# Kernel optimization log

Hardware: AMD Instinct MI355X
Metric: run time of the kernel (lower is better)

## Reference

```python
import math
import jax, jax.numpy as jnp
import numpy as np
from jax import lax

NUM_HEADS = 8


def _conv(x, w, b):
    # 3x3 same-padding conv, NCHW / OIHW
    y = lax.conv_general_dilated(x, w, (1, 1), ((1, 1), (1, 1)),
                                 dimension_numbers=("NCHW", "OIHW", "NCHW"))
    return y + b[None, :, None, None]


def setup_inputs() -> dict:
    key = jax.random.key(0)
    ks = jax.random.split(key, 9)
    C = 16
    s = 0.05
    inp = {"x": jax.random.normal(ks[0], (4, C, 256, 512), jnp.float32)}
    names = ["wq", "bq", "wk", "bk", "wv", "bv", "wo", "bo"]
    for i, n in enumerate(names):
        if n.startswith("w"):
            inp[n] = jax.random.normal(ks[i + 1], (C, C, 3, 3), jnp.float32) * s
        else:
            inp[n] = jax.random.normal(ks[i + 1], (C,), jnp.float32) * s
    return inp


def reference(x, wq, bq, wk, bk, wv, bv, wo, bo):
    b, c, h, w = x.shape
    d = h // NUM_HEADS  # per-head feature dim along the height axis

    def split_heads(t):  # (b,c,h,w) -> (b,c,heads,w,d)
        return t.transpose(0, 1, 3, 2).reshape(b, c, w, NUM_HEADS, d).transpose(0, 1, 3, 2, 4)

    q = split_heads(_conv(x, wq, bq)).astype(jnp.float32)
    k = split_heads(_conv(x, wk, bk)).astype(jnp.float32)
    v = split_heads(_conv(x, wv, bv)).astype(jnp.float32)

    # attention over the width (frame) axis, fp32, scaled by sqrt(h)
    qk = jnp.einsum("bcnwd,bcnud->bcnwu", q, k) / math.sqrt(h)
    a = jnp.einsum("bcnwu,bcnud->bcnwd", jax.nn.softmax(qk, axis=-1), v)

    # (b,c,heads,w,d) -> (b,c,w,h) -> (b,c,h,w)
    a = a.transpose(0, 1, 3, 2, 4).reshape(b, c, w, h).transpose(0, 1, 3, 2)
    return _conv(a, wo, bo)
```

## Files before the change

kernel.cpp:

```cpp
#include <hip/hip_runtime.h>

#define BB 4
#define CC 16
#define HH 256
#define WW 512
#define NHD 8
#define DD 32

typedef __attribute__((ext_vector_type(8))) short s8b;
typedef __attribute__((ext_vector_type(4))) float f32x4;
typedef __attribute__((ext_vector_type(4))) unsigned int u32x4;
typedef __attribute__((ext_vector_type(2))) int i32x2;

__device__ inline unsigned cvtpk(float a, float b) {
    unsigned r;
    asm("v_cvt_pk_bf16_f32 %0, %1, %2" : "=v"(r) : "v"(a), "v"(b));
    return r;
}
__device__ inline f32x4 mfma16(u32x4 a, u32x4 b, f32x4 c) {
    return __builtin_amdgcn_mfma_f32_16x16x32_bf16(
        __builtin_bit_cast(s8b, a), __builtin_bit_cast(s8b, b), c, 0, 0, 0);
}

__global__ __launch_bounds__(64)
void wsetup_kernel(const float* __restrict__ w0, const float* __restrict__ w1,
                   const float* __restrict__ w2, const float* __restrict__ w3,
                   unsigned* __restrict__ wfrag)
{
    const int lane = threadIdx.x;
    const int cv = blockIdx.x;
    const float* wg[4] = {w0, w1, w2, w3};
    const int r = lane & 15, g = lane >> 4;
    const int ci0 = (g & 1) * 8;
    #pragma unroll
    for (int kg = 0; kg < 5; ++kg) {
        int tap = 2*kg + (g >> 1);
        unsigned hi[4], lo[4];
        #pragma unroll
        for (int j = 0; j < 4; ++j) {
            float e0 = 0.f, e1 = 0.f;
            if (tap < 9) {
                e0 = wg[cv][(r*CC + ci0 + 2*j    )*9 + tap];
                e1 = wg[cv][(r*CC + ci0 + 2*j + 1)*9 + tap];
            }
            unsigned h = cvtpk(e0, e1);
            float f0 = __builtin_bit_cast(float, h << 16);
            float f1 = __builtin_bit_cast(float, h & 0xffff0000u);
            hi[j] = h;
            lo[j] = cvtpk(e0 - f0, e1 - f1);
        }
        *(u32x4*)(wfrag + (size_t)(((0*4 + cv)*5 + kg)*64 + lane)*4) =
            (u32x4){hi[0], hi[1], hi[2], hi[3]};
        *(u32x4*)(wfrag + (size_t)(((1*4 + cv)*5 + kg)*64 + lane)*4) =
            (u32x4){lo[0], lo[1], lo[2], lo[3]};
    }
}

template<int NC, int CVB, bool IN_PAIRED, bool OUT_PAIRED, int NTERM>
__global__ __launch_bounds__(256)
void conv_mfma_kernel(const void* __restrict__ xin,
                      const unsigned* __restrict__ wfrag,
                      const float* __restrict__ b0, const float* __restrict__ b1,
                      const float* __restrict__ b2,
                      unsigned* __restrict__ o0, unsigned* __restrict__ o1,
                      unsigned* __restrict__ o2, float* __restrict__ of,
                      float kscale)
{
    constexpr int LC2 = 34, NPX = 18*34;
    constexpr int PXB = (NTERM == 3) ? 64 : 32;
    __shared__ __align__(16) unsigned char xs[NPX*PXB];

    const int tid = threadIdx.x;
    const int bx = blockIdx.x, by = blockIdx.y, bz = blockIdx.z;
    const int lane = tid & 63, wid = tid >> 6;
    const int g = lane >> 4, r = lane & 15;

    u32x4 wh[NC][5], wl[NC][5];
    #pragma unroll
    for (int cv = 0; cv < NC; ++cv)
        #pragma unroll
        for (int kg = 0; kg < 5; ++kg) {
            wh[cv][kg] = *(const u32x4*)(wfrag + (size_t)(((CVB+cv)*5 + kg)*64 + lane)*4);
            if constexpr (NTERM >= 2)
                wl[cv][kg] = *(const u32x4*)(wfrag + (size_t)(((4+CVB+cv)*5 + kg)*64 + lane)*4);
        }
    const float* bg[3] = {b0, b1, b2};
    f32x4 bias[NC];
    #pragma unroll
    for (int cv = 0; cv < NC; ++cv) bias[cv] = *(const f32x4*)(bg[cv] + 4*g);

    const int row0 = by*16 - 1, col0 = bx*32 - 1;
    for (int idx = tid; idx < NPX; idx += 256) {
        int rr = idx / LC2, cc2 = idx - rr*LC2;
        int gr = row0 + rr, gc = col0 + cc2;
        bool ok = (gr >= 0) & (gr < HH) & (gc >= 0) & (gc < WW);
        unsigned hi[8];
        if constexpr (IN_PAIRED) {
            const unsigned* xb = (const unsigned*)xin + (size_t)bz*CC*(HH/2)*WW;
            int grc = gr < 0 ? 0 : (gr > HH-1 ? HH-1 : gr);
            int gcc = gc < 0 ? 0 : (gc > WW-1 ? WW-1 : gc);
            const unsigned* px = xb + (size_t)(grc >> 1)*WW + gcc;
            unsigned wv[16];
            #pragma unroll
            for (int c8 = 0; c8 < 16; ++c8)
                wv[c8] = ok ? px[(size_t)c8*(HH/2)*WW] : 0u;
            const unsigned sel = (grc & 1) ? 0x07060302u : 0x05040100u;
            #pragma unroll
            for (int p = 0; p < 8; ++p)
                hi[p] = __builtin_amdgcn_perm(wv[2*p+1], wv[2*p], sel);
        } else {
            const float* xb = (const float*)xin + (size_t)bz*CC*HH*WW;
            const float* px = xb + (size_t)gr*WW + gc;
            float v0[16];
            #pragma unroll
            for (int c8 = 0; c8 < 16; ++c8) v0[c8] = ok ? px[(size_t)c8*HH*WW] : 0.f;
            #pragma unroll
            for (int p = 0; p < 8; ++p) hi[p] = cvtpk(v0[2*p], v0[2*p+1]);
            if constexpr (NTERM == 3) {
                unsigned lo[8];
                #pragma unroll
                for (int p = 0; p < 8; ++p) {
                    float f0 = __builtin_bit_cast(float, hi[p] << 16);
                    float f1 = __builtin_bit_cast(float, hi[p] & 0xffff0000u);
                    lo[p] = cvtpk(v0[2*p] - f0, v0[2*p+1] - f1);
                }
                unsigned base = (unsigned)idx*64, m = ((unsigned)idx & 3) << 4;
                *(u32x4*)(xs + base + ((32u) ^ m)) = (u32x4){lo[0], lo[1], lo[2], lo[3]};
                *(u32x4*)(xs + base + ((48u) ^ m)) = (u32x4){lo[4], lo[5], lo[6], lo[7]};
            }
        }
        if constexpr (NTERM == 3) {
            unsigned base = (unsigned)idx*64, m = ((unsigned)idx & 3) << 4;
            *(u32x4*)(xs + base + (( 0u) ^ m)) = (u32x4){hi[0], hi[1], hi[2], hi[3]};
            *(u32x4*)(xs + base + ((16u) ^ m)) = (u32x4){hi[4], hi[5], hi[6], hi[7]};
        } else {
            unsigned base = (unsigned)idx*32, m = ((unsigned)idx & 4) << 2;
            *(u32x4*)(xs + base + (( 0u) ^ m)) = (u32x4){hi[0], hi[1], hi[2], hi[3]};
            *(u32x4*)(xs + base + ((16u) ^ m)) = (u32x4){hi[4], hi[5], hi[6], hi[7]};
        }
    }
    __syncthreads();

    int pk_base[5];
    #pragma unroll
    for (int kg = 0; kg < 5; ++kg) {
        int tap = 2*kg + (g >> 1);
        if (tap > 8) tap = 8;
        pk_base[kg] = (tap/3)*LC2 + (tap%3) + r;
    }
    const unsigned sh = (unsigned)(g & 1) << 4;

    auto tile = [&](int hr, int wt, f32x4* acc) {
        const int tb = hr*LC2 + wt*16;
        #pragma unroll
        for (int kg = 0; kg < 5; ++kg) {
            int px = tb + pk_base[kg];
            if constexpr (NTERM == 3) {
                unsigned b_ = (unsigned)px*64, m = ((unsigned)px & 3) << 4;
                u32x4 Bh = *(const u32x4*)(xs + b_ + ( sh        ^ m));
                u32x4 Bl = *(const u32x4*)(xs + b_ + ((sh | 32u) ^ m));
                #pragma unroll
                for (int cv = 0; cv < NC; ++cv) {
                    acc[cv] = mfma16(wh[cv][kg], Bh, acc[cv]);
                    acc[cv] = mfma16(wl[cv][kg], Bh, acc[cv]);
                    acc[cv] = mfma16(wh[cv][kg], Bl, acc[cv]);
                }
            } else {
                unsigned b_ = (unsigned)px*32, m = ((unsigned)px & 4) << 2;
                u32x4 Bh = *(const u32x4*)(xs + b_ + (sh ^ m));
                #pragma unroll
                for (int cv = 0; cv < NC; ++cv) {
                    acc[cv] = mfma16(wh[cv][kg], Bh, acc[cv]);
                    if constexpr (NTERM >= 2)
                        acc[cv] = mfma16(wl[cv][kg], Bh, acc[cv]);
                }
            }
        }
    };

    #pragma unroll 1
    for (int hp = 0; hp < 2; ++hp) {
        const int hrE = 4*wid + 2*hp;
        #pragma unroll 1
        for (int wt = 0; wt < 2; ++wt) {
            const int col = bx*32 + wt*16 + r;
            if constexpr (OUT_PAIRED) {
                f32x4 aE[NC];
                #pragma unroll
                for (int cv = 0; cv < NC; ++cv) aE[cv] = (f32x4){0.f,0.f,0.f,0.f};
                tile(hrE, wt, aE);
                unsigned Ep[NC][2];
                #pragma unroll
                for (int cv = 0; cv < NC; ++cv) {
                    const float sc = (cv == 1) ? kscale : 1.0f;
                    Ep[cv][0] = cvtpk((aE[cv][0] + bias[cv][0])*sc, (aE[cv][1] + bias[cv][1])*sc);
                    Ep[cv][1] = cvtpk((aE[cv][2] + bias[cv][2])*sc, (aE[cv][3] + bias[cv][3])*sc);
                }
                f32x4 aO[NC];
                #pragma unroll
                for (int cv = 0; cv < NC; ++cv) aO[cv] = (f32x4){0.f,0.f,0.f,0.f};
                tile(hrE + 1, wt, aO);
                const int hpix = by*8 + 2*wid + hp;
                #pragma unroll
                for (int cv = 0; cv < NC; ++cv) {
                    const float sc = (cv == 1) ? kscale : 1.0f;
                    unsigned Op0 = cvtpk((aO[cv][0] + bias[cv][0])*sc, (aO[cv][1] + bias[cv][1])*sc);
                    unsigned Op1 = cvtpk((aO[cv][2] + bias[cv][2])*sc, (aO[cv][3] + bias[cv][3])*sc);
                    unsigned wd[4] = {
                        __builtin_amdgcn_perm(Op0, Ep[cv][0], 0x05040100u),
                        __builtin_amdgcn_perm(Op0, Ep[cv][0], 0x07060302u),
                        __builtin_amdgcn_perm(Op1, Ep[cv][1], 0x05040100u),
                        __builtin_amdgcn_perm(Op1, Ep[cv][1], 0x07060302u) };
                    unsigned* op = (cv == 0) ? o0 : (cv == 1) ? o1 : o2;
                    #pragma unroll
                    for (int reg = 0; reg < 4; ++reg)
                        op[((size_t)(bz*CC + 4*g + reg)*(HH/2) + hpix)*WW + col] = wd[reg];
                }
            } else {
                #pragma unroll 1
                for (int e = 0; e < 2; ++e) {
                    f32x4 a0[1] = {(f32x4){0.f,0.f,0.f,0.f}};
                    tile(hrE + e, wt, a0);
                    const int h = by*16 + hrE + e;
                    #pragma unroll
                    for (int reg = 0; reg < 4; ++reg)
                        of[((size_t)(bz*CC + 4*g + reg)*HH + h)*WW + col] =
                            a0[0][reg] + bias[0][reg];
                }
            }
        }
    }
}

__global__ __launch_bounds__(512)
void attn_mfma_kernel(const unsigned* __restrict__ q,
                      const unsigned* __restrict__ k,
                      const unsigned* __restrict__ v,
                      unsigned* __restrict__ apk)
{
    __shared__ __align__(16) unsigned char Kl[WW*DD*2];
    __shared__ __align__(16) unsigned char Vl[DD*WW*2];

    const int s  = blockIdx.x;
    const int n  = s & (NHD-1);
    const int bc = s >> 3;
    const int pbase = (bc*(HH/2) + n*(DD/2)) * WW;
    const unsigned* qg = q + pbase;
    const unsigned* kg = k + pbase;
    const unsigned* vg = v + pbase;
    unsigned* ag = apk + pbase;

    const int tid = threadIdx.x;

    {
        const int key = tid;
        unsigned pk[16];
        #pragma unroll
        for (int dp = 0; dp < 16; ++dp) pk[dp] = kg[(size_t)dp*WW + key];
        #pragma unroll
        for (int j = 0; j < 4; ++j) {
            unsigned off = (unsigned)(key*64 + j*16) ^ ((unsigned)(key&7) << 4);
            *(u32x4*)(Kl + off) = (u32x4){pk[4*j], pk[4*j+1], pk[4*j+2], pk[4*j+3]};
        }
    }
    {
        const int dp = tid >> 5;
        const int k0 = (tid & 31) * 16;
        unsigned rowE[8], rowO[8];
        #pragma unroll
        for (int j = 0; j < 4; ++j) {
            u32x4 U = *(const u32x4*)(vg + (size_t)dp*WW + k0 + 4*j);
            rowE[2*j  ] = __builtin_amdgcn_perm(U[1], U[0], 0x05040100u);
            rowE[2*j+1] = __builtin_amdgcn_perm(U[3], U[2], 0x05040100u);
            rowO[2*j  ] = __builtin_amdgcn_perm(U[1], U[0], 0x07060302u);
            rowO[2*j+1] = __builtin_amdgcn_perm(U[3], U[2], 0x07060302u);
        }
        const int d0 = 2*dp, d1 = 2*dp + 1;
        const unsigned bE = (unsigned)(d0*1024 + k0*2);
        const unsigned bO = (unsigned)(d1*1024 + k0*2);
        const unsigned mE = ((unsigned)d0 & 7u) << 4;
        const unsigned mO = ((unsigned)d1 & 7u) << 4;
        *(u32x4*)(Vl + ((bE     ) ^ mE)) = (u32x4){rowE[0], rowE[1], rowE[4], rowE[5]};
        *(u32x4*)(Vl + ((bE + 16) ^ mE)) = (u32x4){rowE[2], rowE[3], rowE[6], rowE[7]};
        *(u32x4*)(Vl + ((bO     ) ^ mO)) = (u32x4){rowO[0], rowO[1], rowO[4], rowO[5]};
        *(u32x4*)(Vl + ((bO + 16) ^ mO)) = (u32x4){rowO[2], rowO[3], rowO[6], rowO[7]};
    }

    const int wid  = tid >> 6;
    const int lane = tid & 63;
    const int g = lane >> 4;
    const int r = lane & 15;
    const int w0 = wid * 64;

    u32x4 qf[4];
    #pragma unroll
    for (int rf = 0; rf < 4; ++rf) {
        const int row = w0 + rf*16 + r;
        unsigned pq[4];
        #pragma unroll
        for (int jj = 0; jj < 4; ++jj)
            pq[jj] = qg[(size_t)(4*g + jj)*WW + row];
        qf[rf] = (u32x4){pq[0], pq[1], pq[2], pq[3]};
    }

    __syncthreads();

    const u32x4 vones = (r == 0)
        ? (u32x4){0x3F803F80u, 0x3F803F80u, 0x3F803F80u, 0x3F803F80u}
        : (u32x4){0u, 0u, 0u, 0u};

    f32x4 oacc[4][2];
    f32x4 lacc[4];
    #pragma unroll
    for (int qi = 0; qi < 4; ++qi) {
        oacc[qi][0] = (f32x4){0.f,0.f,0.f,0.f};
        oacc[qi][1] = (f32x4){0.f,0.f,0.f,0.f};
        lacc[qi]    = (f32x4){0.f,0.f,0.f,0.f};
    }

    #pragma unroll 1
    for (int j0 = 0; j0 < WW; j0 += 32) {
        u32x4 kf[2];
        #pragma unroll
        for (int cf = 0; cf < 2; ++cf) {
            const int key = j0 + cf*16 + r;
            unsigned off = (unsigned)(key*64 + g*16) ^ ((unsigned)(key&7) << 4);
            kf[cf] = *(const u32x4*)(Kl + off);
        }
        u32x4 vf[2];
        #pragma unroll
        for (int cfd = 0; cfd < 2; ++cfd) {
            const int d = r + 16*cfd;
            unsigned off = (unsigned)(d*1024 + (j0 + 8*g)*2) ^ ((unsigned)(d&7) << 4);
            vf[cfd] = *(const u32x4*)(Vl + off);
        }

        f32x4 sacc[4][2];
        #pragma unroll
        for (int qi = 0; qi < 4; ++qi) {
            sacc[qi][0] = mfma16(kf[0], qf[qi], (f32x4){0.f,0.f,0.f,0.f});
            sacc[qi][1] = mfma16(kf[1], qf[qi], (f32x4){0.f,0.f,0.f,0.f});
        }

        #pragma unroll
        for (int qi = 0; qi < 4; ++qi) {
            float p0 = __builtin_amdgcn_exp2f(sacc[qi][0][0]);
            float p1 = __builtin_amdgcn_exp2f(sacc[qi][0][1]);
            float p2 = __builtin_amdgcn_exp2f(sacc[qi][0][2]);
            float p3 = __builtin_amdgcn_exp2f(sacc[qi][0][3]);
            float p4 = __builtin_amdgcn_exp2f(sacc[qi][1][0]);
            float p5 = __builtin_amdgcn_exp2f(sacc[qi][1][1]);
            float p6 = __builtin_amdgcn_exp2f(sacc[qi][1][2]);
            float p7 = __builtin_amdgcn_exp2f(sacc[qi][1][3]);
            unsigned Aw = cvtpk(p0, p1);
            unsigned Bw = cvtpk(p2, p3);
            unsigned Cw = cvtpk(p4, p5);
            unsigned Dw = cvtpk(p6, p7);
            i32x2 w02 = __builtin_amdgcn_permlane32_swap((int)Aw, (int)Cw, false, false);
            i32x2 w13 = __builtin_amdgcn_permlane32_swap((int)Bw, (int)Dw, false, false);
            u32x4 pa = (u32x4){ (unsigned)w02[0], (unsigned)w13[0],
                                (unsigned)w02[1], (unsigned)w13[1] };
            oacc[qi][0] = mfma16(vf[0], pa, oacc[qi][0]);
            oacc[qi][1] = mfma16(vf[1], pa, oacc[qi][1]);
            lacc[qi]    = mfma16(vones, pa, lacc[qi]);
        }
    }

    #pragma unroll
    for (int qi = 0; qi < 4; ++qi) {
        float l = __shfl(lacc[qi][0], r);
        float inv = 1.0f / l;
        const int qcol = w0 + qi*16 + r;
        #pragma unroll
        for (int cfd = 0; cfd < 2; ++cfd) {
            const int dpair = 8*cfd + 2*g;
            unsigned P0 = cvtpk(oacc[qi][cfd][0]*inv, oacc[qi][cfd][1]*inv);
            unsigned P1 = cvtpk(oacc[qi][cfd][2]*inv, oacc[qi][cfd][3]*inv);
            ag[(size_t)(dpair    )*WW + qcol] = P0;
            ag[(size_t)(dpair + 1)*WW + qcol] = P1;
        }
    }
}

extern "C" void kernel_launch(void* const* d_in, const int* in_sizes, int n_in,
                              void* d_out, int out_size, void* d_ws, size_t ws_size,
                              hipStream_t stream) {
    (void)in_sizes; (void)n_in; (void)out_size; (void)ws_size;
    const float* x  = (const float*)d_in[0];
    const float* wq = (const float*)d_in[1];
    const float* bq = (const float*)d_in[2];
    const float* wk = (const float*)d_in[3];
    const float* bk = (const float*)d_in[4];
    const float* wv = (const float*)d_in[5];
    const float* bv = (const float*)d_in[6];
    const float* wo = (const float*)d_in[7];
    const float* bo = (const float*)d_in[8];
    float* out = (float*)d_out;

    const float SC = 0.0625f * 1.44269504088896340736f;

    const size_t S = (size_t)BB*CC*HH*WW;
    unsigned* apk  = (unsigned*)d_ws;
    unsigned* qpk  = apk + S/2;
    unsigned* kpk  = qpk + S/2;
    unsigned* vpk  = kpk + S/2;
    unsigned* wfrag = vpk + S/2;

    wsetup_kernel<<<dim3(4), 64, 0, stream>>>(wq, wk, wv, wo, wfrag);
    dim3 cgrid(WW/32, HH/16, BB);
    conv_mfma_kernel<3, 0, false, true, 1><<<cgrid, 256, 0, stream>>>(
        x, wfrag, bq, bk, bv, qpk, kpk, vpk, nullptr, SC);
    attn_mfma_kernel<<<dim3(512), 512, 0, stream>>>(qpk, kpk, vpk, apk);
    conv_mfma_kernel<1, 3, true, false, 2><<<cgrid, 256, 0, stream>>>(
        apk, wfrag, bo, bo, bo, nullptr, nullptr, nullptr, out, 1.0f);
}
```

Measured before the change: 80.57 us.

## Pre-pack input into channel-last bf16 layout before QKV conv

Adds a kernel that transposes the fp32 NCHW input through shared memory into a channel-last bf16 layout with 16 channels per pixel. The QKV conv then loads each halo pixel with two 16-byte reads instead of 16 strided scalar fp32 loads plus conversion. This costs an extra kernel launch and an extra write and read of the packed input in exchange for coalesced, vectorised conv input loads.

```diff
diff --git a/kernel.cpp b/kernel.cpp
--- a/kernel.cpp
+++ b/kernel.cpp
@@ -56,7 +56,41 @@
     }
 }
 
-template<int NC, int CVB, bool IN_PAIRED, bool OUT_PAIRED, int NTERM>
+__global__ __launch_bounds__(256)
+void xpack_kernel(const float* __restrict__ x, unsigned* __restrict__ xcl)
+{
+    __shared__ float xsf[8][16][68];
+    const int tid = threadIdx.x;
+    const int bx = blockIdx.x, by = blockIdx.y, bz = blockIdx.z;
+    const float* xb = x + (size_t)bz*CC*HH*WW + (size_t)(by*8)*WW + bx*64;
+
+    #pragma unroll
+    for (int k = 0; k < 8; ++k) {
+        int idx = tid + k*256;
+        int ci  = idx >> 7;
+        int rem = idx & 127;
+        int hh  = rem >> 4;
+        int qq  = rem & 15;
+        f32x4 v = *(const f32x4*)(xb + (size_t)ci*HH*WW + (size_t)hh*WW + qq*4);
+        *(f32x4*)&xsf[hh][ci][qq*4] = v;
+    }
+    __syncthreads();
+
+    #pragma unroll
+    for (int k = 0; k < 2; ++k) {
+        int p  = tid + k*256;
+        int hh = p >> 6, ww = p & 63;
+        unsigned pk[8];
+        #pragma unroll
+        for (int q = 0; q < 8; ++q)
+            pk[q] = cvtpk(xsf[hh][2*q][ww], xsf[hh][2*q+1][ww]);
+        unsigned* op = xcl + ((size_t)(bz*HH + by*8 + hh)*WW + bx*64 + ww)*8;
+        *(u32x4*)(op    ) = (u32x4){pk[0], pk[1], pk[2], pk[3]};
+        *(u32x4*)(op + 4) = (u32x4){pk[4], pk[5], pk[6], pk[7]};
+    }
+}
+
+template<int NC, int CVB, int INMODE, bool OUT_PAIRED, int NTERM>
 __global__ __launch_bounds__(256)
 void conv_mfma_kernel(const void* __restrict__ xin,
                       const unsigned* __restrict__ wfrag,
@@ -94,8 +128,21 @@
         int rr = idx / LC2, cc2 = idx - rr*LC2;
         int gr = row0 + rr, gc = col0 + cc2;
         bool ok = (gr >= 0) & (gr < HH) & (gc >= 0) & (gc < WW);
+        if constexpr (INMODE == 2) {
+            const unsigned* xb = (const unsigned*)xin + (size_t)bz*HH*WW*8;
+            int grc = gr < 0 ? 0 : (gr > HH-1 ? HH-1 : gr);
+            int gcc = gc < 0 ? 0 : (gc > WW-1 ? WW-1 : gc);
+            const unsigned* px = xb + ((size_t)grc*WW + gcc)*8;
+            u32x4 A = *(const u32x4*)(px);
+            u32x4 Bv = *(const u32x4*)(px + 4);
+            if (!ok) { A = (u32x4){0,0,0,0}; Bv = (u32x4){0,0,0,0}; }
+            unsigned base = (unsigned)idx*32, m = ((unsigned)idx & 4) << 2;
+            *(u32x4*)(xs + base + (( 0u) ^ m)) = A;
+            *(u32x4*)(xs + base + ((16u) ^ m)) = Bv;
+            continue;
+        }
         unsigned hi[8];
-        if constexpr (IN_PAIRED) {
+        if constexpr (INMODE == 1) {
             const unsigned* xb = (const unsigned*)xin + (size_t)bz*CC*(HH/2)*WW;
             int grc = gr < 0 ? 0 : (gr > HH-1 ? HH-1 : gr);
             int gcc = gc < 0 ? 0 : (gc > WW-1 ? WW-1 : gc);
@@ -108,7 +155,7 @@
             #pragma unroll
             for (int p = 0; p < 8; ++p)
                 hi[p] = __builtin_amdgcn_perm(wv[2*p+1], wv[2*p], sel);
-        } else {
+        } else if constexpr (INMODE == 0) {
             const float* xb = (const float*)xin + (size_t)bz*CC*HH*WW;
             const float* px = xb + (size_t)gr*WW + gc;
             float v0[16];
@@ -404,13 +451,15 @@
     unsigned* qpk  = apk + S/2;
     unsigned* kpk  = qpk + S/2;
     unsigned* vpk  = kpk + S/2;
-    unsigned* wfrag = vpk + S/2;
+    unsigned* xcl  = vpk + S/2;
+    unsigned* wfrag = xcl + S/2;
 
     wsetup_kernel<<<dim3(4), 64, 0, stream>>>(wq, wk, wv, wo, wfrag);
+    xpack_kernel<<<dim3(WW/64, HH/8, BB), 256, 0, stream>>>(x, xcl);
     dim3 cgrid(WW/32, HH/16, BB);
-    conv_mfma_kernel<3, 0, false, true, 1><<<cgrid, 256, 0, stream>>>(
-        x, wfrag, bq, bk, bv, qpk, kpk, vpk, nullptr, SC);
+    conv_mfma_kernel<3, 0, 2, true, 1><<<cgrid, 256, 0, stream>>>(
+        xcl, wfrag, bq, bk, bv, qpk, kpk, vpk, nullptr, SC);
     attn_mfma_kernel<<<dim3(512), 512, 0, stream>>>(qpk, kpk, vpk, apk);
-    conv_mfma_kernel<1, 3, true, false, 2><<<cgrid, 256, 0, stream>>>(
+    conv_mfma_kernel<1, 3, 1, false, 2><<<cgrid, 256, 0, stream>>>(
         apk, wfrag, bo, bo, bo, nullptr, nullptr, nullptr, out, 1.0f);
 }
```

Result: faster. 77.15 us (-4.2%).
